# Optimization experiments

Hardware: AMD Instinct MI355X
Metric: run time of the kernel (lower is better)

## Reference

```python
import jax, jax.numpy as jnp
import numpy as np


def setup_inputs() -> dict:
    key = jax.random.key(0)
    k1, k2 = jax.random.split(key)
    embeddings = jax.random.normal(k1, (8, 128, 8192), dtype=jnp.float32)
    codebooks = jax.random.normal(k2, (8, 1024, 128), dtype=jnp.float32)
    return {"embeddings": embeddings, "codebooks": codebooks}


def reference(embeddings, codebooks):
    # embeddings: [B, D, T] -> [B, T, D]
    x = jnp.transpose(embeddings, (0, 2, 1))

    def step(residual, embed):
        # residual: [B, T, D]; embed: [K, D]
        # squared euclidean distance (argmin over -dist == argmax of dist in torch code)
        dist = (
            jnp.sum(residual * residual, axis=-1, keepdims=True)
            - 2.0 * jnp.einsum("btd,kd->btk", residual, embed)
            + jnp.sum(embed * embed, axis=-1)
        )  # [B, T, K]
        idx = jnp.argmin(dist, axis=-1)  # [B, T]
        quantized = embed[idx]  # [B, T, D]
        return residual - quantized, (idx, quantized)

    _, (indices, quants) = jax.lax.scan(step, x, codebooks)
    # indices: [Q, B, T]; quants: [Q, B, T, D]
    quantized_out = jnp.transpose(jnp.sum(quants, axis=0), (0, 2, 1))  # [B, D, T]
    return indices, quantized_out
```

## Files before the change

kernel.cpp:

```cpp
#include <hip/hip_runtime.h>
#include <float.h>

#define NQ 8
#define NB 8
#define ND 128
#define NT 8192
#define NK 1024
#define TTILE 64
#define ESTR 136
#define TAU 2e-3f

typedef _Float16 half8 __attribute__((ext_vector_type(8)));
typedef float f32x4 __attribute__((ext_vector_type(4)));

__device__ __forceinline__ float np_sumsq_strided(const float* a, int stride) {
#pragma clang fp contract(off)
    float r[8];
    #pragma unroll
    for (int j = 0; j < 8; ++j) { float v = a[j * stride]; r[j] = v * v; }
    #pragma unroll
    for (int i = 1; i < 16; ++i) {
        #pragma unroll
        for (int j = 0; j < 8; ++j) {
            float v = a[(i * 8 + j) * stride];
            r[j] = r[j] + v * v;
        }
    }
    return ((r[0] + r[1]) + (r[2] + r[3])) + ((r[4] + r[5]) + (r[6] + r[7]));
}

__global__ void e2_kernel(const float* __restrict__ cb, float* __restrict__ e2) {
    int i = blockIdx.x * blockDim.x + threadIdx.x;
    e2[i] = np_sumsq_strided(cb + (size_t)i * ND, 1);
}

__global__ __launch_bounds__(256, 2) void rvq_kernel(
    const float* __restrict__ emb, const float* __restrict__ cbs,
    const float* __restrict__ e2ws, float* __restrict__ out)
{
    __shared__ float res[ND * TTILE];
    __shared__ _Float16 ebh[64 * ESTR];
    __shared__ _Float16 ebl[64 * ESTR];
    __shared__ float e2q[NK];
    __shared__ float mb1[2][TTILE], mb2[2][TTILE];
    __shared__ int   mi1[2][TTILE];
    __shared__ int   idx_lds[TTILE];
    __shared__ unsigned long long flagmask;
    __shared__ float wbd[4]; __shared__ int wbi[4];

    const int tid  = threadIdx.x;
    const int lane = tid & 63;
    const int wv   = tid >> 6;
    const int tg   = wv >> 1;
    const int ch   = wv & 1;
    const int c16  = lane & 15;
    const int g4   = lane >> 4;

    const int bidx = blockIdx.x;
    const int b  = bidx >> 7;
    const int t0 = (bidx & 127) * TTILE;
    const float* x = emb + (size_t)b * ND * NT + t0;

    {
        int d = tid >> 1, toff = (tid & 1) * 32;
        #pragma unroll
        for (int j = 0; j < 8; ++j)
            *(float4*)&res[d * TTILE + toff + j * 4] = *(const float4*)(x + d * NT + toff + j * 4);
    }
    __syncthreads();

    float* out_idx = out;
    float* out_qt  = out + (size_t)NQ * NB * NT;

    for (int q = 0; q < NQ; ++q) {
        const float* cb = cbs + (size_t)q * NK * ND;

        half8 aH[2][4], aL[2][4];
        #pragma unroll
        for (int mt = 0; mt < 2; ++mt) {
            int tok = tg * 32 + mt * 16 + c16;
            #pragma unroll
            for (int kk = 0; kk < 4; ++kk) {
                int k0 = kk * 32 + g4 * 8;
                half8 hh, hl;
                #pragma unroll
                for (int j = 0; j < 8; ++j) {
                    float v = res[(k0 + j) * TTILE + tok];
                    _Float16 h = (_Float16)v;
                    hh[j] = h;
                    hl[j] = (_Float16)(v - (float)h);
                }
                aH[mt][kk] = hh; aL[mt][kk] = hl;
            }
        }
        #pragma unroll
        for (int c = 0; c < 4; ++c) e2q[c * 256 + tid] = e2ws[q * NK + c * 256 + tid];

        float B1[8], B2[8]; int I1[8];
        #pragma unroll
        for (int s = 0; s < 8; ++s) { B1[s] = FLT_MAX; B2[s] = FLT_MAX; I1[s] = 0; }

        for (int r = 0; r < 16; ++r) {
            __syncthreads();
            {
                int row = tid >> 2, seg = tid & 3;
                int gcode = (row >> 5) * 512 + r * 32 + (row & 31);
                const float* gs = cb + (size_t)gcode * ND + seg * 32;
                _Float16* dh = &ebh[row * ESTR + seg * 32];
                _Float16* dl = &ebl[row * ESTR + seg * 32];
                #pragma unroll
                for (int u = 0; u < 4; ++u) {
                    float4 v0 = *(const float4*)(gs + u * 8);
                    float4 v1 = *(const float4*)(gs + u * 8 + 4);
                    float vv[8] = {v0.x, v0.y, v0.z, v0.w, v1.x, v1.y, v1.z, v1.w};
                    half8 hh, hl;
                    #pragma unroll
                    for (int j = 0; j < 8; ++j) {
                        _Float16 h = (_Float16)vv[j];
                        hh[j] = h;
                        hl[j] = (_Float16)(vv[j] - (float)h);
                    }
                    *(half8*)(dh + u * 8) = hh;
                    *(half8*)(dl + u * 8) = hl;
                }
            }
            __syncthreads();

            #pragma unroll
            for (int cblk = 0; cblk < 2; ++cblk) {
                int crow = ch * 32 + cblk * 16 + c16;
                half8 bH[4], bL[4];
                #pragma unroll
                for (int kk = 0; kk < 4; ++kk) {
                    bH[kk] = *(const half8*)&ebh[crow * ESTR + kk * 32 + g4 * 8];
                    bL[kk] = *(const half8*)&ebl[crow * ESTR + kk * 32 + g4 * 8];
                }
                int gk = ch * 512 + r * 32 + cblk * 16 + c16;
                float e2v = e2q[gk];

                f32x4 acc0 = {0.f, 0.f, 0.f, 0.f};
                f32x4 acc1 = {0.f, 0.f, 0.f, 0.f};
                #pragma unroll
                for (int s = 0; s < 4; ++s) {
                    #pragma unroll
                    for (int kk = 0; kk < 4; ++kk) {
                        half8 a0 = (s & 2) ? aL[0][kk] : aH[0][kk];
                        half8 a1 = (s & 2) ? aL[1][kk] : aH[1][kk];
                        half8 bb = (s & 1) ? bL[kk] : bH[kk];
                        acc0 = __builtin_amdgcn_mfma_f32_16x16x32_f16(a0, bb, acc0, 0, 0, 0);
                        acc1 = __builtin_amdgcn_mfma_f32_16x16x32_f16(a1, bb, acc1, 0, 0, 0);
                    }
                }
                #pragma unroll
                for (int j = 0; j < 4; ++j) {
                    float d0 = fmaf(-2.f, acc0[j], e2v);
                    if (d0 < B1[j])      { B2[j] = B1[j]; B1[j] = d0; I1[j] = gk; }
                    else if (d0 < B2[j]) { B2[j] = d0; }
                    float d1 = fmaf(-2.f, acc1[j], e2v);
                    if (d1 < B1[4 + j])      { B2[4 + j] = B1[4 + j]; B1[4 + j] = d1; I1[4 + j] = gk; }
                    else if (d1 < B2[4 + j]) { B2[4 + j] = d1; }
                }
            }
        }

        #pragma unroll
        for (int s = 0; s < 8; ++s) {
            #pragma unroll
            for (int off = 1; off < 16; off <<= 1) {
                float ob1 = __shfl_xor(B1[s], off, 16);
                float ob2 = __shfl_xor(B2[s], off, 16);
                int   oi  = __shfl_xor(I1[s], off, 16);
                if (ob1 < B1[s] || (ob1 == B1[s] && oi < I1[s])) {
                    B2[s] = fminf(B1[s], ob2); B1[s] = ob1; I1[s] = oi;
                } else {
                    B2[s] = fminf(ob1, B2[s]);
                }
            }
        }
        if (c16 == 0) {
            #pragma unroll
            for (int mt = 0; mt < 2; ++mt)
                #pragma unroll
                for (int j = 0; j < 4; ++j) {
                    int tl = tg * 32 + mt * 16 + g4 * 4 + j;
                    int s = mt * 4 + j;
                    mb1[ch][tl] = B1[s]; mb2[ch][tl] = B2[s]; mi1[ch][tl] = I1[s];
                }
        }
        __syncthreads();

        if (tid < TTILE) {
            float b1 = mb1[0][tid], b2 = mb2[0][tid]; int i1 = mi1[0][tid];
            float c1 = mb1[1][tid], c2 = mb2[1][tid]; int j1 = mi1[1][tid];
            if (c1 < b1) { b2 = fminf(b1, c2); b1 = c1; i1 = j1; }
            else         { b2 = fminf(c1, b2); }
            idx_lds[tid] = i1;
            bool flag = (b2 - b1) < TAU;
            unsigned long long fm = __ballot(flag);
            if (tid == 0) flagmask = fm;
        }
        __syncthreads();

        unsigned long long mask = flagmask;
        while (mask) {
            int t = __ffsll((long long)mask) - 1; mask &= mask - 1;
            float r2t = np_sumsq_strided(&res[t], TTILE);
            float bd = FLT_MAX; int bi = 0;
            #pragma unroll
            for (int c = 0; c < 4; ++c) {
                int k = tid + 256 * c;
                const float* er = cb + (size_t)k * ND;
                float s = 0.f;
                #pragma unroll 8
                for (int d = 0; d < ND; ++d)
                    s = fmaf(res[d * TTILE + t], er[d], s);
                float dist;
                {
                #pragma clang fp contract(off)
                    dist = (r2t - 2.0f * s) + e2q[k];
                }
                if (dist < bd) { bd = dist; bi = k; }
            }
            #pragma unroll
            for (int off = 32; off >= 1; off >>= 1) {
                float od = __shfl_xor(bd, off);
                int   oi = __shfl_xor(bi, off);
                if (od < bd || (od == bd && oi < bi)) { bd = od; bi = oi; }
            }
            if (lane == 0) { wbd[wv] = bd; wbi[wv] = bi; }
            __syncthreads();
            if (tid == 0) {
                #pragma unroll
                for (int w = 1; w < 4; ++w)
                    if (wbd[w] < bd || (wbd[w] == bd && wbi[w] < bi)) { bd = wbd[w]; bi = wbi[w]; }
                idx_lds[t] = bi;
            }
            __syncthreads();
        }

        if (tid < TTILE)
            out_idx[(size_t)q * NB * NT + (size_t)b * NT + t0 + tid] = (float)idx_lds[tid];
        {
            int t = tid & 63, grp = tid >> 6;
            int ki = idx_lds[t];
            const float* erow = cb + (size_t)ki * ND + grp * 32;
            #pragma unroll
            for (int j = 0; j < 32; ++j)
                res[(grp * 32 + j) * TTILE + t] = res[(grp * 32 + j) * TTILE + t] - erow[j];
        }
        __syncthreads();
    }

    {
        int d = tid >> 1, toff = (tid & 1) * 32;
        float* o = out_qt + (size_t)b * ND * NT + t0;
        #pragma unroll
        for (int j = 0; j < 8; ++j) {
            float4 xv = *(const float4*)(x + d * NT + toff + j * 4);
            float4 rv = *(const float4*)&res[d * TTILE + toff + j * 4];
            float4 ov = {xv.x - rv.x, xv.y - rv.y, xv.z - rv.z, xv.w - rv.w};
            *(float4*)(o + d * NT + toff + j * 4) = ov;
        }
    }
}

extern "C" void kernel_launch(void* const* d_in, const int* in_sizes, int n_in,
                              void* d_out, int out_size, void* d_ws, size_t ws_size,
                              hipStream_t stream) {
    const float* emb = (const float*)d_in[0];
    const float* cbs = (const float*)d_in[1];
    float* out = (float*)d_out;
    float* e2ws = (float*)d_ws;

    e2_kernel<<<NQ * NK / 256, 256, 0, stream>>>(cbs, e2ws);
    rvq_kernel<<<NB * NT / TTILE, 256, 0, stream>>>(emb, cbs, e2ws, out);
}
```

Measured before the change: 1.209 ms.

## Precompute fp16 hi/lo codebook planes and stream via direct global-to-LDS loads

A new prep kernel splits each codebook tile into fp16 hi/lo planes laid out exactly as the LDS tile, once per launch. The main kernel then copies each tile with global_load_lds instead of every block reconverting fp32 codebooks. It also drops the lo*lo MFMA term, going from 4 to 3 products per k-step. The cost is an extra kernel launch and more workspace, plus a small precision loss near argmin ties.

```diff
diff --git a/kernel.cpp b/kernel.cpp
--- a/kernel.cpp
+++ b/kernel.cpp
@@ -8,6 +8,7 @@
 #define NK 1024
 #define TTILE 64
 #define ESTR 136
+#define PLANE_HALVES (64 * ESTR)
 #define TAU 2e-3f
 
 typedef _Float16 half8 __attribute__((ext_vector_type(8)));
@@ -34,13 +35,39 @@
     e2[i] = np_sumsq_strided(cb + (size_t)i * ND, 1);
 }
 
+__global__ void prep_kernel(const float* __restrict__ cbs, _Float16* __restrict__ planes) {
+    int qr = blockIdx.x;
+    int q = qr >> 4, r = qr & 15;
+    int tid = threadIdx.x;
+    int sr = tid >> 2, seg = tid & 3;
+    int gcode = (sr >> 5) * 512 + r * 32 + (sr & 31);
+    const float* gs = cbs + ((size_t)q * NK + gcode) * ND + seg * 32;
+    _Float16* dh = planes + (size_t)qr * 2 * PLANE_HALVES + sr * ESTR + seg * 32;
+    _Float16* dl = dh + PLANE_HALVES;
+    #pragma unroll
+    for (int u = 0; u < 4; ++u) {
+        float4 v0 = *(const float4*)(gs + u * 8);
+        float4 v1 = *(const float4*)(gs + u * 8 + 4);
+        float vv[8] = {v0.x, v0.y, v0.z, v0.w, v1.x, v1.y, v1.z, v1.w};
+        half8 hh, hl;
+        #pragma unroll
+        for (int j = 0; j < 8; ++j) {
+            _Float16 h = (_Float16)vv[j];
+            hh[j] = h;
+            hl[j] = (_Float16)(vv[j] - (float)h);
+        }
+        *(half8*)(dh + u * 8) = hh;
+        *(half8*)(dl + u * 8) = hl;
+    }
+}
+
 __global__ __launch_bounds__(256, 2) void rvq_kernel(
     const float* __restrict__ emb, const float* __restrict__ cbs,
-    const float* __restrict__ e2ws, float* __restrict__ out)
+    const float* __restrict__ e2ws, const _Float16* __restrict__ planes,
+    float* __restrict__ out)
 {
     __shared__ float res[ND * TTILE];
-    __shared__ _Float16 ebh[64 * ESTR];
-    __shared__ _Float16 ebl[64 * ESTR];
+    __shared__ _Float16 eb[2 * PLANE_HALVES];
     __shared__ float e2q[NK];
     __shared__ float mb1[2][TTILE], mb2[2][TTILE];
     __shared__ int   mi1[2][TTILE];
@@ -103,25 +130,13 @@
         for (int r = 0; r < 16; ++r) {
             __syncthreads();
             {
-                int row = tid >> 2, seg = tid & 3;
-                int gcode = (row >> 5) * 512 + r * 32 + (row & 31);
-                const float* gs = cb + (size_t)gcode * ND + seg * 32;
-                _Float16* dh = &ebh[row * ESTR + seg * 32];
-                _Float16* dl = &ebl[row * ESTR + seg * 32];
-                #pragma unroll
-                for (int u = 0; u < 4; ++u) {
-                    float4 v0 = *(const float4*)(gs + u * 8);
-                    float4 v1 = *(const float4*)(gs + u * 8 + 4);
-                    float vv[8] = {v0.x, v0.y, v0.z, v0.w, v1.x, v1.y, v1.z, v1.w};
-                    half8 hh, hl;
-                    #pragma unroll
-                    for (int j = 0; j < 8; ++j) {
-                        _Float16 h = (_Float16)vv[j];
-                        hh[j] = h;
-                        hl[j] = (_Float16)(vv[j] - (float)h);
-                    }
-                    *(half8*)(dh + u * 8) = hh;
-                    *(half8*)(dl + u * 8) = hl;
+                const char* src = (const char*)(planes + (size_t)(q * 16 + r) * 2 * PLANE_HALVES);
+                for (int c = wv; c < 34; c += 4) {
+                    const char* g = src + c * 1024 + (lane << 4);
+                    char* l = (char*)eb + c * 1024;
+                    __builtin_amdgcn_global_load_lds(
+                        (const __attribute__((address_space(1))) unsigned int*)g,
+                        (__attribute__((address_space(3))) unsigned int*)l, 16, 0, 0);
                 }
             }
             __syncthreads();
@@ -132,8 +147,8 @@
                 half8 bH[4], bL[4];
                 #pragma unroll
                 for (int kk = 0; kk < 4; ++kk) {
-                    bH[kk] = *(const half8*)&ebh[crow * ESTR + kk * 32 + g4 * 8];
-                    bL[kk] = *(const half8*)&ebl[crow * ESTR + kk * 32 + g4 * 8];
+                    bH[kk] = *(const half8*)&eb[crow * ESTR + kk * 32 + g4 * 8];
+                    bL[kk] = *(const half8*)&eb[PLANE_HALVES + crow * ESTR + kk * 32 + g4 * 8];
                 }
                 int gk = ch * 512 + r * 32 + cblk * 16 + c16;
                 float e2v = e2q[gk];
@@ -141,15 +156,19 @@
                 f32x4 acc0 = {0.f, 0.f, 0.f, 0.f};
                 f32x4 acc1 = {0.f, 0.f, 0.f, 0.f};
                 #pragma unroll
-                for (int s = 0; s < 4; ++s) {
-                    #pragma unroll
-                    for (int kk = 0; kk < 4; ++kk) {
-                        half8 a0 = (s & 2) ? aL[0][kk] : aH[0][kk];
-                        half8 a1 = (s & 2) ? aL[1][kk] : aH[1][kk];
-                        half8 bb = (s & 1) ? bL[kk] : bH[kk];
-                        acc0 = __builtin_amdgcn_mfma_f32_16x16x32_f16(a0, bb, acc0, 0, 0, 0);
-                        acc1 = __builtin_amdgcn_mfma_f32_16x16x32_f16(a1, bb, acc1, 0, 0, 0);
-                    }
+                for (int kk = 0; kk < 4; ++kk) {
+                    acc0 = __builtin_amdgcn_mfma_f32_16x16x32_f16(aH[0][kk], bH[kk], acc0, 0, 0, 0);
+                    acc1 = __builtin_amdgcn_mfma_f32_16x16x32_f16(aH[1][kk], bH[kk], acc1, 0, 0, 0);
+                }
+                #pragma unroll
+                for (int kk = 0; kk < 4; ++kk) {
+                    acc0 = __builtin_amdgcn_mfma_f32_16x16x32_f16(aH[0][kk], bL[kk], acc0, 0, 0, 0);
+                    acc1 = __builtin_amdgcn_mfma_f32_16x16x32_f16(aH[1][kk], bL[kk], acc1, 0, 0, 0);
+                }
+                #pragma unroll
+                for (int kk = 0; kk < 4; ++kk) {
+                    acc0 = __builtin_amdgcn_mfma_f32_16x16x32_f16(aL[0][kk], bH[kk], acc0, 0, 0, 0);
+                    acc1 = __builtin_amdgcn_mfma_f32_16x16x32_f16(aL[1][kk], bH[kk], acc1, 0, 0, 0);
                 }
                 #pragma unroll
                 for (int j = 0; j < 4; ++j) {
@@ -271,7 +290,9 @@
     const float* cbs = (const float*)d_in[1];
     float* out = (float*)d_out;
     float* e2ws = (float*)d_ws;
+    _Float16* planes = (_Float16*)((char*)d_ws + 32768);
 
     e2_kernel<<<NQ * NK / 256, 256, 0, stream>>>(cbs, e2ws);
-    rvq_kernel<<<NB * NT / TTILE, 256, 0, stream>>>(emb, cbs, e2ws, out);
-}
+    prep_kernel<<<NQ * 16, 256, 0, stream>>>(cbs, planes);
+    rvq_kernel<<<NB * NT / TTILE, 256, 0, stream>>>(emb, cbs, e2ws, planes, out);
+}
```

After: 978.7 us. 1.24x faster.
